# Optimization experiments

Measured on AMD Instinct MI355X. Metric: run time of the kernel, lower is better.

Reference implementation:

```python
import jax, jax.numpy as jnp
import numpy as np

NHEAD = 16


def corrcoef(X, Y):
    # X, Y: [..., S, D]; Pearson correlation between rows of X and rows of Y
    X = X - X.mean(-1, keepdims=True)
    Y = Y - Y.mean(-1, keepdims=True)
    c = jnp.einsum('...id,...jd->...ij', X, Y)            # [..., S, S]
    d = jnp.einsum('...id,...id->...i', X, Y)             # diagonal of c
    stddev = jnp.sqrt(d)
    c = c / stddev[..., :, None]
    c = c / stddev[..., None, :]
    c = jnp.clip(c, -1.0, 1.0)
    return jnp.where(jnp.isnan(c), 0.0, c)


def setup_inputs() -> dict:
    key = jax.random.key(0)
    k1, k2, k3 = jax.random.split(key, 3)
    T, B, D = 2048, 2, 1024
    query = jax.random.normal(k1, (T, B, D), dtype=jnp.float32)
    W_qkv = jax.random.normal(k2, (3 * D, D), dtype=jnp.float32) * (1.0 / np.sqrt(D))
    b_qkv = jax.random.normal(k3, (3 * D,), dtype=jnp.float32) * 0.01
    return {"query": query, "W_qkv": W_qkv, "b_qkv": b_qkv}


def reference(query, W_qkv, b_qkv):
    T, B, D = query.shape
    hd = D // NHEAD
    qkv = query @ W_qkv.T + b_qkv                          # [T, B, 3D]
    q, k, v = jnp.split(qkv, 3, axis=-1)

    def to_bhsd(x):
        return x.reshape(T, B, NHEAD, hd).transpose(1, 2, 0, 3)  # [B, H, S, hd]

    q, k, v = to_bhsd(q), to_bhsd(k), to_bhsd(v)
    corr = corrcoef(q, k)                                   # [B, H, S, S]
    corr = jax.nn.softmax(corr, axis=-1)                    # eval: dropout_p = 0
    return corr @ v                                         # [B, H, S, hd]
```

## Files before the change

kernel.cpp:

```cpp
#include <hip/hip_runtime.h>

#define S 2048
#define D 1024
#define NH 16
#define HD 64
#define N3 3072
#define M 4096

typedef short s16x8 __attribute__((ext_vector_type(8)));
typedef _Float16 f16x8 __attribute__((ext_vector_type(8)));
typedef float f32x4 __attribute__((ext_vector_type(4)));
typedef unsigned int u32;

__device__ __forceinline__ unsigned short f2bf(float f) {
  unsigned u = __builtin_bit_cast(unsigned, f);
  u += 0x7fffu + ((u >> 16) & 1u);
  return (unsigned short)(u >> 16);
}
__device__ __forceinline__ float bf2f(unsigned short h) {
  return __builtin_bit_cast(float, (unsigned)h << 16);
}

__device__ __forceinline__ float wsum(float v) {
  #pragma unroll
  for (int m = 1; m < 64; m <<= 1) v += __shfl_xor(v, m, 64);
  return v;
}

__device__ __forceinline__ void gload_lds16(const unsigned short* g, unsigned short* l) {
  __builtin_amdgcn_global_load_lds(
      (const __attribute__((address_space(1))) u32*)g,
      (__attribute__((address_space(3))) u32*)l, 16, 0, 0);
}

__global__ __launch_bounds__(256) void split_k(const float* __restrict__ q,
                                               const float* __restrict__ w,
                                               unsigned short* __restrict__ A1,
                                               unsigned short* __restrict__ A2,
                                               unsigned short* __restrict__ W1,
                                               unsigned short* __restrict__ W2) {
  const size_t gid = (size_t)blockIdx.x * 256 + threadIdx.x;
  const size_t NA = (size_t)M * D / 4;
  float4 x;
  unsigned short* p1; unsigned short* p2; size_t qi; float scale;
  if (gid < NA) {
    qi = gid;  x = ((const float4*)q)[qi];
    p1 = A1; p2 = A2; scale = 64.f;
  } else {
    qi = gid - NA;  x = ((const float4*)w)[qi];
    p1 = W1; p2 = W2; scale = 1024.f;
  }
  float e[4] = {x.x * scale, x.y * scale, x.z * scale, x.w * scale};
  unsigned short h1[4], h2[4];
  #pragma unroll
  for (int i = 0; i < 4; ++i) {
    _Float16 a = (_Float16)e[i];
    float r = e[i] - (float)a;
    _Float16 b = (_Float16)r;
    h1[i] = __builtin_bit_cast(unsigned short, a);
    h2[i] = __builtin_bit_cast(unsigned short, b);
  }
  *(ushort4*)&p1[qi * 4] = make_ushort4(h1[0], h1[1], h1[2], h1[3]);
  *(ushort4*)&p2[qi * 4] = make_ushort4(h2[0], h2[1], h2[2], h2[3]);
}

__global__ __launch_bounds__(256) void gemm_mfma(const unsigned short* __restrict__ A1,
                                                 const unsigned short* __restrict__ A2,
                                                 const unsigned short* __restrict__ W1,
                                                 const unsigned short* __restrict__ W2,
                                                 const float* __restrict__ bias,
                                                 float* __restrict__ C) {
  __shared__ unsigned short As[128 * 64];
  __shared__ unsigned short Bs[128 * 64];
  const int tid = threadIdx.x;
  const int w = tid >> 6, l = tid & 63;
  const int lo = l & 15, hi = l >> 4;
  const int n0 = blockIdx.x * 128, m0 = blockIdx.y * 128;
  const int wr = w >> 1, wc = w & 1;

  const int nseg = (n0 >= 2048) ? 1 : 3;

  const int srow = (tid >> 3) & 31;
  const int skc = tid & 7;

  f32x4 acc[4][4];
  #pragma unroll
  for (int mi = 0; mi < 4; ++mi)
    #pragma unroll
    for (int nj = 0; nj < 4; ++nj) acc[mi][nj] = (f32x4){0.f, 0.f, 0.f, 0.f};

  for (int s = 0; s < 3; ++s) {
    if (s >= nseg) break;
    const unsigned short* Ab;
    const unsigned short* Bb;
    switch (s) {
      case 0: Ab = A1; Bb = W1; break;
      case 1: Ab = A2; Bb = W1; break;
      default: Ab = A1; Bb = W2; break;
    }
    Ab += (size_t)m0 * D;
    Bb += (size_t)n0 * D;

    for (int k0 = 0; k0 < D; k0 += 64) {
      __syncthreads();
      #pragma unroll
      for (int c = 0; c < 4; ++c) {
        const int row = c * 32 + srow;
        const int koct = skc ^ (row & 7);
        gload_lds16(Ab + (size_t)row * D + k0 + koct * 8,
                    As + c * 2048 + w * 512);
        gload_lds16(Bb + (size_t)row * D + k0 + koct * 8,
                    Bs + c * 2048 + w * 512);
      }
      __syncthreads();

      f16x8 af[4][2], bf[4][2];
      #pragma unroll
      for (int mi = 0; mi < 4; ++mi)
        #pragma unroll
        for (int ks = 0; ks < 2; ++ks) {
          const int row = wr * 64 + mi * 16 + lo;
          const int koct = (ks * 4 + hi) ^ (lo & 7);
          af[mi][ks] = *(const f16x8*)&As[row * 64 + koct * 8];
        }
      #pragma unroll
      for (int nj = 0; nj < 4; ++nj)
        #pragma unroll
        for (int ks = 0; ks < 2; ++ks) {
          const int row = wc * 64 + nj * 16 + lo;
          const int koct = (ks * 4 + hi) ^ (lo & 7);
          bf[nj][ks] = *(const f16x8*)&Bs[row * 64 + koct * 8];
        }
      #pragma unroll
      for (int mi = 0; mi < 4; ++mi)
        #pragma unroll
        for (int nj = 0; nj < 4; ++nj)
          #pragma unroll
          for (int ks = 0; ks < 2; ++ks)
            acc[mi][nj] = __builtin_amdgcn_mfma_f32_16x16x32_f16(
                af[mi][ks], bf[nj][ks], acc[mi][nj], 0, 0, 0);
    }
  }

  #pragma unroll
  for (int mi = 0; mi < 4; ++mi)
    #pragma unroll
    for (int nj = 0; nj < 4; ++nj) {
      const int n = n0 + wc * 64 + nj * 16 + lo;
      const float bj = bias[n];
      #pragma unroll
      for (int r = 0; r < 4; ++r) {
        const int m = m0 + wr * 64 + mi * 16 + hi * 4 + r;
        C[(size_t)m * N3 + n] = acc[mi][nj][r] * (1.f / 65536.f) + bj;
      }
    }
}

__global__ __launch_bounds__(256) void stats_k(const float* __restrict__ qkv,
                                               unsigned short* __restrict__ qhi,
                                               unsigned short* __restrict__ qlo,
                                               unsigned short* __restrict__ khi,
                                               unsigned short* __restrict__ klo,
                                               unsigned short* __restrict__ vt,
                                               float* __restrict__ rs) {
  __shared__ unsigned short VsT[64][65];
  const int tt = blockIdx.x, bh = blockIdx.y;
  const int b = bh >> 4, h = bh & 15;
  const int w = threadIdx.x >> 6, l = threadIdx.x & 63;

  for (int rr = 0; rr < 16; ++rr) {
    const int t = tt * 64 + w * 16 + rr;
    const size_t base = (size_t)(t * 2 + b) * N3 + h * HD;
    const float q = qkv[base + l];
    const float k = qkv[base + D + l];
    const float v = qkv[base + 2 * D + l];
    const float qm = wsum(q) * (1.f / 64.f);
    const float km = wsum(k) * (1.f / 64.f);
    const float qcv = q - qm, kcv = k - km;
    const float d = wsum(qcv * kcv);
    float rv = 0.f;
    if (d > 0.f) {
      rv = rsqrtf(d);
      rv = rv * (1.5f - 0.5f * d * rv * rv);
    }
    const size_t ro = ((size_t)bh * S + t) * HD + l;
    const unsigned short qh = f2bf(qcv);
    const unsigned short kh = f2bf(kcv);
    qhi[ro] = qh;  qlo[ro] = f2bf(qcv - bf2f(qh));
    khi[ro] = kh;  klo[ro] = f2bf(kcv - bf2f(kh));
    if (l == 0) rs[(size_t)bh * S + t] = rv;
    VsT[l][w * 16 + rr] = f2bf(v);
  }
  __syncthreads();
  const int dd = threadIdx.x >> 2, seg = threadIdx.x & 3;
  unsigned pk[8];
  #pragma unroll
  for (int e = 0; e < 8; ++e) {
    unsigned l2 = VsT[dd][seg * 16 + 2 * e];
    unsigned h2 = VsT[dd][seg * 16 + 2 * e + 1];
    pk[e] = l2 | (h2 << 16);
  }
  unsigned short* dst = vt + ((size_t)bh * HD + dd) * S + tt * 64 + seg * 16;
  *(uint4*)dst       = make_uint4(pk[0], pk[1], pk[2], pk[3]);
  *(uint4*)(dst + 8) = make_uint4(pk[4], pk[5], pk[6], pk[7]);
}

__global__ __launch_bounds__(256) void attn_k(const unsigned short* __restrict__ qhi,
                                              const unsigned short* __restrict__ qlo,
                                              const unsigned short* __restrict__ khi,
                                              const unsigned short* __restrict__ klo,
                                              const unsigned short* __restrict__ vt,
                                              const float* __restrict__ rs,
                                              float* __restrict__ out) {
  __shared__ unsigned short Kh[64 * 64];
  __shared__ unsigned short Kl[64 * 64];
  __shared__ unsigned short Vsm[64 * 64];
  __shared__ unsigned short Ps[128 * 64];

  const int tid = threadIdx.x;
  const int w = tid >> 6, l = tid & 63;
  const int lo = l & 15, hi = l >> 4;

  const int wgid = blockIdx.x;
  const int orig = (wgid & 7) * 64 + (wgid >> 3);
  const int bh = orig >> 4, qt = orig & 15;

  const unsigned short* qhb = qhi + (size_t)bh * S * HD;
  const unsigned short* qlb = qlo + (size_t)bh * S * HD;
  const unsigned short* khb = khi + (size_t)bh * S * HD;
  const unsigned short* klb = klo + (size_t)bh * S * HD;
  const unsigned short* vbase = vt + (size_t)bh * HD * S;
  const float* rbase = rs + (size_t)bh * S;
  const int qrow0 = qt * 128 + w * 32;

  const int srow8 = l >> 3;
  const int sg = (l & 7) ^ srow8;

  s16x8 aqh[2][2], aql[2][2];
  #pragma unroll
  for (int mi = 0; mi < 2; ++mi)
    #pragma unroll
    for (int ks = 0; ks < 2; ++ks) {
      const size_t off = (size_t)(qrow0 + mi * 16 + lo) * HD + ks * 32 + hi * 8;
      aqh[mi][ks] = *(const s16x8*)(qhb + off);
      aql[mi][ks] = *(const s16x8*)(qlb + off);
    }

  float rsq[2][4];
  #pragma unroll
  for (int mi = 0; mi < 2; ++mi)
    #pragma unroll
    for (int r = 0; r < 4; ++r)
      rsq[mi][r] = rbase[qrow0 + mi * 16 + hi * 4 + r];

  f32x4 oacc[2][4];
  float den[2][4];
  #pragma unroll
  for (int mi = 0; mi < 2; ++mi)
    #pragma unroll
    for (int nd = 0; nd < 4; ++nd) {
      oacc[mi][nd] = (f32x4){0.f, 0.f, 0.f, 0.f};
      den[mi][nd] = 0.f;
    }

  for (int j0 = 0; j0 < S; j0 += 64) {
    __syncthreads();
    #pragma unroll
    for (int c = 0; c < 2; ++c) {
      const int row = c * 32 + w * 8 + srow8;
      const size_t kgo = (size_t)(j0 + row) * HD + sg * 8;
      const int dst = c * 2048 + w * 512;
      gload_lds16(khb + kgo, Kh + dst);
      gload_lds16(klb + kgo, Kl + dst);
      gload_lds16(vbase + (size_t)row * S + j0 + sg * 8, Vsm + dst);
    }
    float rjv[4];
    #pragma unroll
    for (int nj = 0; nj < 4; ++nj) rjv[nj] = rbase[j0 + nj * 16 + lo];
    __syncthreads();

    #pragma unroll
    for (int mi = 0; mi < 2; ++mi) {
      #pragma unroll
      for (int nj = 0; nj < 4; ++nj) {
        f32x4 acc = (f32x4){0.f, 0.f, 0.f, 0.f};
        #pragma unroll
        for (int ks = 0; ks < 2; ++ks) {
          const int off = (nj * 16 + lo) * 64 + (((ks * 4 + hi) ^ (lo & 7)) << 3);
          s16x8 bkh = *(const s16x8*)&Kh[off];
          s16x8 bkl = *(const s16x8*)&Kl[off];
          acc = __builtin_amdgcn_mfma_f32_16x16x32_bf16(aqh[mi][ks], bkh, acc, 0, 0, 0);
          acc = __builtin_amdgcn_mfma_f32_16x16x32_bf16(aqh[mi][ks], bkl, acc, 0, 0, 0);
          acc = __builtin_amdgcn_mfma_f32_16x16x32_bf16(aql[mi][ks], bkh, acc, 0, 0, 0);
        }
        #pragma unroll
        for (int r = 0; r < 4; ++r) {
          float c = acc[r] * rsq[mi][r] * rjv[nj];
          c = fminf(1.f, fmaxf(-1.f, c));
          const float e = __expf(c);
          den[mi][r] += e;
          const int pr = w * 32 + mi * 16 + hi * 4 + r;
          Ps[pr * 64 + ((((nj * 2) + (lo >> 3)) ^ (pr & 7)) << 3) + (lo & 7)] = f2bf(e);
        }
      }
    }

    #pragma unroll
    for (int mi = 0; mi < 2; ++mi) {
      const int prow = w * 32 + mi * 16 + lo;
      s16x8 pa0 = *(const s16x8*)&Ps[prow * 64 + ((hi ^ (lo & 7)) << 3)];
      s16x8 pa1 = *(const s16x8*)&Ps[prow * 64 + (((4 + hi) ^ (lo & 7)) << 3)];
      #pragma unroll
      for (int nd = 0; nd < 4; ++nd) {
        const int vrow = nd * 16 + lo;
        s16x8 bv0 = *(const s16x8*)&Vsm[vrow * 64 + ((hi ^ (lo & 7)) << 3)];
        s16x8 bv1 = *(const s16x8*)&Vsm[vrow * 64 + (((4 + hi) ^ (lo & 7)) << 3)];
        oacc[mi][nd] = __builtin_amdgcn_mfma_f32_16x16x32_bf16(pa0, bv0, oacc[mi][nd], 0, 0, 0);
        oacc[mi][nd] = __builtin_amdgcn_mfma_f32_16x16x32_bf16(pa1, bv1, oacc[mi][nd], 0, 0, 0);
      }
    }
  }

  #pragma unroll
  for (int mi = 0; mi < 2; ++mi)
    #pragma unroll
    for (int r = 0; r < 4; ++r) {
      float dsum = den[mi][r];
      dsum += __shfl_xor(dsum, 1, 64);
      dsum += __shfl_xor(dsum, 2, 64);
      dsum += __shfl_xor(dsum, 4, 64);
      dsum += __shfl_xor(dsum, 8, 64);
      den[mi][r] = 1.f / dsum;
    }
  #pragma unroll
  for (int mi = 0; mi < 2; ++mi)
    #pragma unroll
    for (int nd = 0; nd < 4; ++nd)
      #pragma unroll
      for (int r = 0; r < 4; ++r) {
        const size_t row = (size_t)bh * S + qrow0 + mi * 16 + hi * 4 + r;
        out[row * HD + nd * 16 + lo] = oacc[mi][nd][r] * den[mi][r];
      }
}

extern "C" void kernel_launch(void* const* d_in, const int* in_sizes, int n_in,
                              void* d_out, int out_size, void* d_ws, size_t ws_size,
                              hipStream_t stream) {
  const float* query = (const float*)d_in[0];
  const float* W     = (const float*)d_in[1];
  const float* bias  = (const float*)d_in[2];
  float* out = (float*)d_out;
  char* ws = (char*)d_ws;

  float*          qkv = (float*)ws;
  unsigned short* A1 = (unsigned short*)(ws + 50331648);
  unsigned short* A2 = (unsigned short*)(ws + 58720256);
  unsigned short* W1 = (unsigned short*)(ws + 67108864);
  unsigned short* W2 = (unsigned short*)(ws + 73400320);
  unsigned short* qhi = (unsigned short*)(ws + 50331648);
  unsigned short* qlo = (unsigned short*)(ws + 58720256);
  unsigned short* khi = (unsigned short*)(ws + 67108864);
  unsigned short* klo = (unsigned short*)(ws + 75497472);
  unsigned short* vt  = (unsigned short*)(ws + 83886080);
  float*          rsb = (float*)(ws + 92274688);

  split_k  <<<dim3(7168), 256, 0, stream>>>(query, W, A1, A2, W1, W2);
  gemm_mfma<<<dim3(24, 32), 256, 0, stream>>>(A1, A2, W1, W2, bias, qkv);
  stats_k  <<<dim3(32, 32), 256, 0, stream>>>(qkv, qhi, qlo, khi, klo, vt, rsb);
  attn_k   <<<dim3(512), 256, 0, stream>>>(qhi, qlo, khi, klo, vt, rsb, out);
}
```

Baseline: 192.4 us.

## Prescale q/k by row rstd and split attention across eight 16-row waves

The stats kernel now multiplies the centered q and k rows by the per-row reciprocal stddev before the bf16 hi/lo split. This lets the attention kernel drop the rs buffer, its per-tile loads and the per-element rescaling. The attention kernel moves to 512 threads, with each of 8 waves handling 16 query rows instead of 32, and each thread now issues a single K/V tile load. The goal is more resident waves and fewer registers per wave to hide latency, but each K/V fragment read from LDS now feeds half as many MFMAs.

```diff
diff --git a/kernel.cpp b/kernel.cpp
--- a/kernel.cpp
+++ b/kernel.cpp
@@ -161,8 +161,7 @@
                                                unsigned short* __restrict__ qlo,
                                                unsigned short* __restrict__ khi,
                                                unsigned short* __restrict__ klo,
-                                               unsigned short* __restrict__ vt,
-                                               float* __restrict__ rs) {
+                                               unsigned short* __restrict__ vt) {
   __shared__ unsigned short VsT[64][65];
   const int tt = blockIdx.x, bh = blockIdx.y;
   const int b = bh >> 4, h = bh & 15;
@@ -183,12 +182,12 @@
       rv = rsqrtf(d);
       rv = rv * (1.5f - 0.5f * d * rv * rv);
     }
+    const float qn = qcv * rv, kn = kcv * rv;
     const size_t ro = ((size_t)bh * S + t) * HD + l;
-    const unsigned short qh = f2bf(qcv);
-    const unsigned short kh = f2bf(kcv);
-    qhi[ro] = qh;  qlo[ro] = f2bf(qcv - bf2f(qh));
-    khi[ro] = kh;  klo[ro] = f2bf(kcv - bf2f(kh));
-    if (l == 0) rs[(size_t)bh * S + t] = rv;
+    const unsigned short qh = f2bf(qn);
+    const unsigned short kh = f2bf(kn);
+    qhi[ro] = qh;  qlo[ro] = f2bf(qn - bf2f(qh));
+    khi[ro] = kh;  klo[ro] = f2bf(kn - bf2f(kh));
     VsT[l][w * 16 + rr] = f2bf(v);
   }
   __syncthreads();
@@ -205,12 +204,11 @@
   *(uint4*)(dst + 8) = make_uint4(pk[4], pk[5], pk[6], pk[7]);
 }
 
-__global__ __launch_bounds__(256) void attn_k(const unsigned short* __restrict__ qhi,
+__global__ __launch_bounds__(512) void attn_k(const unsigned short* __restrict__ qhi,
                                               const unsigned short* __restrict__ qlo,
                                               const unsigned short* __restrict__ khi,
                                               const unsigned short* __restrict__ klo,
                                               const unsigned short* __restrict__ vt,
-                                              const float* __restrict__ rs,
                                               float* __restrict__ out) {
   __shared__ unsigned short Kh[64 * 64];
   __shared__ unsigned short Kl[64 * 64];
@@ -230,84 +228,58 @@
   const unsigned short* khb = khi + (size_t)bh * S * HD;
   const unsigned short* klb = klo + (size_t)bh * S * HD;
   const unsigned short* vbase = vt + (size_t)bh * HD * S;
-  const float* rbase = rs + (size_t)bh * S;
-  const int qrow0 = qt * 128 + w * 32;
-
-  const int srow8 = l >> 3;
-  const int sg = (l & 7) ^ srow8;
-
-  s16x8 aqh[2][2], aql[2][2];
-  #pragma unroll
-  for (int mi = 0; mi < 2; ++mi)
-    #pragma unroll
-    for (int ks = 0; ks < 2; ++ks) {
-      const size_t off = (size_t)(qrow0 + mi * 16 + lo) * HD + ks * 32 + hi * 8;
-      aqh[mi][ks] = *(const s16x8*)(qhb + off);
-      aql[mi][ks] = *(const s16x8*)(qlb + off);
-    }
-
-  float rsq[2][4];
-  #pragma unroll
-  for (int mi = 0; mi < 2; ++mi)
-    #pragma unroll
-    for (int r = 0; r < 4; ++r)
-      rsq[mi][r] = rbase[qrow0 + mi * 16 + hi * 4 + r];
-
-  f32x4 oacc[2][4];
-  float den[2][4];
-  #pragma unroll
-  for (int mi = 0; mi < 2; ++mi)
-    #pragma unroll
-    for (int nd = 0; nd < 4; ++nd) {
-      oacc[mi][nd] = (f32x4){0.f, 0.f, 0.f, 0.f};
-      den[mi][nd] = 0.f;
-    }
+  const int qrow0 = qt * 128 + w * 16;
+
+  const int srow = tid >> 3;
+  const int sg = (tid & 7) ^ (srow & 7);
+
+  s16x8 aqh[2], aql[2];
+  #pragma unroll
+  for (int ks = 0; ks < 2; ++ks) {
+    const size_t off = (size_t)(qrow0 + lo) * HD + ks * 32 + hi * 8;
+    aqh[ks] = *(const s16x8*)(qhb + off);
+    aql[ks] = *(const s16x8*)(qlb + off);
+  }
+
+  f32x4 oacc[4];
+  float den[4];
+  #pragma unroll
+  for (int nd = 0; nd < 4; ++nd) { oacc[nd] = (f32x4){0.f, 0.f, 0.f, 0.f}; den[nd] = 0.f; }
 
   for (int j0 = 0; j0 < S; j0 += 64) {
     __syncthreads();
+    {
+      const size_t kgo = (size_t)(j0 + srow) * HD + sg * 8;
+      gload_lds16(khb + kgo, Kh + w * 512);
+      gload_lds16(klb + kgo, Kl + w * 512);
+      gload_lds16(vbase + (size_t)srow * S + j0 + sg * 8, Vsm + w * 512);
+    }
+    __syncthreads();
+
     #pragma unroll
-    for (int c = 0; c < 2; ++c) {
-      const int row = c * 32 + w * 8 + srow8;
-      const size_t kgo = (size_t)(j0 + row) * HD + sg * 8;
-      const int dst = c * 2048 + w * 512;
-      gload_lds16(khb + kgo, Kh + dst);
-      gload_lds16(klb + kgo, Kl + dst);
-      gload_lds16(vbase + (size_t)row * S + j0 + sg * 8, Vsm + dst);
-    }
-    float rjv[4];
-    #pragma unroll
-    for (int nj = 0; nj < 4; ++nj) rjv[nj] = rbase[j0 + nj * 16 + lo];
-    __syncthreads();
-
-    #pragma unroll
-    for (int mi = 0; mi < 2; ++mi) {
-      #pragma unroll
-      for (int nj = 0; nj < 4; ++nj) {
-        f32x4 acc = (f32x4){0.f, 0.f, 0.f, 0.f};
-        #pragma unroll
-        for (int ks = 0; ks < 2; ++ks) {
-          const int off = (nj * 16 + lo) * 64 + (((ks * 4 + hi) ^ (lo & 7)) << 3);
-          s16x8 bkh = *(const s16x8*)&Kh[off];
-          s16x8 bkl = *(const s16x8*)&Kl[off];
-          acc = __builtin_amdgcn_mfma_f32_16x16x32_bf16(aqh[mi][ks], bkh, acc, 0, 0, 0);
-          acc = __builtin_amdgcn_mfma_f32_16x16x32_bf16(aqh[mi][ks], bkl, acc, 0, 0, 0);
-          acc = __builtin_amdgcn_mfma_f32_16x16x32_bf16(aql[mi][ks], bkh, acc, 0, 0, 0);
-        }
-        #pragma unroll
-        for (int r = 0; r < 4; ++r) {
-          float c = acc[r] * rsq[mi][r] * rjv[nj];
-          c = fminf(1.f, fmaxf(-1.f, c));
-          const float e = __expf(c);
-          den[mi][r] += e;
-          const int pr = w * 32 + mi * 16 + hi * 4 + r;
-          Ps[pr * 64 + ((((nj * 2) + (lo >> 3)) ^ (pr & 7)) << 3) + (lo & 7)] = f2bf(e);
-        }
-      }
-    }
-
-    #pragma unroll
-    for (int mi = 0; mi < 2; ++mi) {
-      const int prow = w * 32 + mi * 16 + lo;
+    for (int nj = 0; nj < 4; ++nj) {
+      f32x4 acc = (f32x4){0.f, 0.f, 0.f, 0.f};
+      #pragma unroll
+      for (int ks = 0; ks < 2; ++ks) {
+        const int off = (nj * 16 + lo) * 64 + (((ks * 4 + hi) ^ (lo & 7)) << 3);
+        s16x8 bkh = *(const s16x8*)&Kh[off];
+        s16x8 bkl = *(const s16x8*)&Kl[off];
+        acc = __builtin_amdgcn_mfma_f32_16x16x32_bf16(aqh[ks], bkh, acc, 0, 0, 0);
+        acc = __builtin_amdgcn_mfma_f32_16x16x32_bf16(aqh[ks], bkl, acc, 0, 0, 0);
+        acc = __builtin_amdgcn_mfma_f32_16x16x32_bf16(aql[ks], bkh, acc, 0, 0, 0);
+      }
+      #pragma unroll
+      for (int r = 0; r < 4; ++r) {
+        float c = fminf(1.f, fmaxf(-1.f, acc[r]));
+        const float e = __expf(c);
+        den[r] += e;
+        const int pr = w * 16 + hi * 4 + r;
+        Ps[pr * 64 + ((((nj * 2) + (lo >> 3)) ^ (pr & 7)) << 3) + (lo & 7)] = f2bf(e);
+      }
+    }
+
+    {
+      const int prow = w * 16 + lo;
       s16x8 pa0 = *(const s16x8*)&Ps[prow * 64 + ((hi ^ (lo & 7)) << 3)];
       s16x8 pa1 = *(const s16x8*)&Ps[prow * 64 + (((4 + hi) ^ (lo & 7)) << 3)];
       #pragma unroll
@@ -315,32 +287,28 @@
         const int vrow = nd * 16 + lo;
         s16x8 bv0 = *(const s16x8*)&Vsm[vrow * 64 + ((hi ^ (lo & 7)) << 3)];
         s16x8 bv1 = *(const s16x8*)&Vsm[vrow * 64 + (((4 + hi) ^ (lo & 7)) << 3)];
-        oacc[mi][nd] = __builtin_amdgcn_mfma_f32_16x16x32_bf16(pa0, bv0, oacc[mi][nd], 0, 0, 0);
-        oacc[mi][nd] = __builtin_amdgcn_mfma_f32_16x16x32_bf16(pa1, bv1, oacc[mi][nd], 0, 0, 0);
-      }
-    }
-  }
-
-  #pragma unroll
-  for (int mi = 0; mi < 2; ++mi)
+        oacc[nd] = __builtin_amdgcn_mfma_f32_16x16x32_bf16(pa0, bv0, oacc[nd], 0, 0, 0);
+        oacc[nd] = __builtin_amdgcn_mfma_f32_16x16x32_bf16(pa1, bv1, oacc[nd], 0, 0, 0);
+      }
+    }
+  }
+
+  #pragma unroll
+  for (int r = 0; r < 4; ++r) {
+    float dsum = den[r];
+    dsum += __shfl_xor(dsum, 1, 64);
+    dsum += __shfl_xor(dsum, 2, 64);
+    dsum += __shfl_xor(dsum, 4, 64);
+    dsum += __shfl_xor(dsum, 8, 64);
+    den[r] = 1.f / dsum;
+  }
+  #pragma unroll
+  for (int nd = 0; nd < 4; ++nd)
     #pragma unroll
     for (int r = 0; r < 4; ++r) {
-      float dsum = den[mi][r];
-      dsum += __shfl_xor(dsum, 1, 64);
-      dsum += __shfl_xor(dsum, 2, 64);
-      dsum += __shfl_xor(dsum, 4, 64);
-      dsum += __shfl_xor(dsum, 8, 64);
-      den[mi][r] = 1.f / dsum;
-    }
-  #pragma unroll
-  for (int mi = 0; mi < 2; ++mi)
-    #pragma unroll
-    for (int nd = 0; nd < 4; ++nd)
-      #pragma unroll
-      for (int r = 0; r < 4; ++r) {
-        const size_t row = (size_t)bh * S + qrow0 + mi * 16 + hi * 4 + r;
-        out[row * HD + nd * 16 + lo] = oacc[mi][nd][r] * den[mi][r];
-      }
+      const size_t row = (size_t)bh * S + qrow0 + hi * 4 + r;
+      out[row * HD + nd * 16 + lo] = oacc[nd][r] * den[r];
+    }
 }
 
 extern "C" void kernel_launch(void* const* d_in, const int* in_sizes, int n_in,
@@ -362,10 +330,9 @@
   unsigned short* khi = (unsigned short*)(ws + 67108864);
   unsigned short* klo = (unsigned short*)(ws + 75497472);
   unsigned short* vt  = (unsigned short*)(ws + 83886080);
-  float*          rsb = (float*)(ws + 92274688);
 
   split_k  <<<dim3(7168), 256, 0, stream>>>(query, W, A1, A2, W1, W2);
   gemm_mfma<<<dim3(24, 32), 256, 0, stream>>>(A1, A2, W1, W2, bias, qkv);
-  stats_k  <<<dim3(32, 32), 256, 0, stream>>>(qkv, qhi, qlo, khi, klo, vt, rsb);
-  attn_k   <<<dim3(512), 256, 0, stream>>>(qhi, qlo, khi, klo, vt, rsb, out);
-}
+  stats_k  <<<dim3(32, 32), 256, 0, stream>>>(qkv, qhi, qlo, khi, klo, vt);
+  attn_k   <<<dim3(512), 512, 0, stream>>>(qhi, qlo, khi, klo, vt, out);
+}
```

Result: faster. 177.7 us (-7.6%).

## Keep softmax probabilities in registers using transposed 32x32 MFMA and fp16 V

Applied to the files above, without the earlier changes.

Rewrites the attention inner loop to use 32x32x16 MFMAs that compute S^T (K as the A operand, Q as B). The exponentiated probabilities are then packed to fp16 and redistributed with a cross-half-wave shuffle so they feed the PV MFMA directly from registers, with no round trip through the Ps shared-memory buffer. V is now stored as fp16 instead of bf16 to match, and the per-column row scales are loaded into LDS once per tile. This removes the LDS writes and reads for P and one barrier-free bank-conflict source, at the cost of extra shuffles and a changed output write pattern.

```diff
diff --git a/kernel.cpp b/kernel.cpp
--- a/kernel.cpp
+++ b/kernel.cpp
@@ -10,7 +10,9 @@
 typedef short s16x8 __attribute__((ext_vector_type(8)));
 typedef _Float16 f16x8 __attribute__((ext_vector_type(8)));
 typedef float f32x4 __attribute__((ext_vector_type(4)));
+typedef float f32x16 __attribute__((ext_vector_type(16)));
 typedef unsigned int u32;
+typedef u32 u32x4 __attribute__((ext_vector_type(4)));
 
 __device__ __forceinline__ unsigned short f2bf(float f) {
   unsigned u = __builtin_bit_cast(unsigned, f);
@@ -20,6 +22,10 @@
 __device__ __forceinline__ float bf2f(unsigned short h) {
   return __builtin_bit_cast(float, (unsigned)h << 16);
 }
+__device__ __forceinline__ unsigned short f2h(float f) {
+  _Float16 h = (_Float16)f;
+  return __builtin_bit_cast(unsigned short, h);
+}
 
 __device__ __forceinline__ float wsum(float v) {
   #pragma unroll
@@ -31,6 +37,11 @@
   __builtin_amdgcn_global_load_lds(
       (const __attribute__((address_space(1))) u32*)g,
       (__attribute__((address_space(3))) u32*)l, 16, 0, 0);
+}
+__device__ __forceinline__ void gload_lds4(const float* g, float* l) {
+  __builtin_amdgcn_global_load_lds(
+      (const __attribute__((address_space(1))) u32*)g,
+      (__attribute__((address_space(3))) u32*)l, 4, 0, 0);
 }
 
 __global__ __launch_bounds__(256) void split_k(const float* __restrict__ q,
@@ -189,7 +200,7 @@
     qhi[ro] = qh;  qlo[ro] = f2bf(qcv - bf2f(qh));
     khi[ro] = kh;  klo[ro] = f2bf(kcv - bf2f(kh));
     if (l == 0) rs[(size_t)bh * S + t] = rv;
-    VsT[l][w * 16 + rr] = f2bf(v);
+    VsT[l][w * 16 + rr] = f2h(v);
   }
   __syncthreads();
   const int dd = threadIdx.x >> 2, seg = threadIdx.x & 3;
@@ -215,11 +226,13 @@
   __shared__ unsigned short Kh[64 * 64];
   __shared__ unsigned short Kl[64 * 64];
   __shared__ unsigned short Vsm[64 * 64];
-  __shared__ unsigned short Ps[128 * 64];
+  __shared__ float Rsl[64];
 
   const int tid = threadIdx.x;
   const int w = tid >> 6, l = tid & 63;
-  const int lo = l & 15, hi = l >> 4;
+  const int lq = l & 31;
+  const int h = l >> 5;
+  const int l7 = l & 7;
 
   const int wgid = blockIdx.x;
   const int orig = (wgid & 7) * 64 + (wgid >> 3);
@@ -233,114 +246,103 @@
   const float* rbase = rs + (size_t)bh * S;
   const int qrow0 = qt * 128 + w * 32;
 
-  const int srow8 = l >> 3;
-  const int sg = (l & 7) ^ srow8;
-
-  s16x8 aqh[2][2], aql[2][2];
-  #pragma unroll
-  for (int mi = 0; mi < 2; ++mi)
-    #pragma unroll
-    for (int ks = 0; ks < 2; ++ks) {
-      const size_t off = (size_t)(qrow0 + mi * 16 + lo) * HD + ks * 32 + hi * 8;
-      aqh[mi][ks] = *(const s16x8*)(qhb + off);
-      aql[mi][ks] = *(const s16x8*)(qlb + off);
-    }
-
-  float rsq[2][4];
-  #pragma unroll
-  for (int mi = 0; mi < 2; ++mi)
-    #pragma unroll
-    for (int r = 0; r < 4; ++r)
-      rsq[mi][r] = rbase[qrow0 + mi * 16 + hi * 4 + r];
-
-  f32x4 oacc[2][4];
-  float den[2][4];
-  #pragma unroll
-  for (int mi = 0; mi < 2; ++mi)
-    #pragma unroll
-    for (int nd = 0; nd < 4; ++nd) {
-      oacc[mi][nd] = (f32x4){0.f, 0.f, 0.f, 0.f};
-      den[mi][nd] = 0.f;
-    }
+  const int srow3 = l >> 3;
+  const int sg = l7 ^ srow3;
+
+  s16x8 qfh[4], qfl[4];
+  #pragma unroll
+  for (int kc = 0; kc < 4; ++kc) {
+    const size_t off = (size_t)(qrow0 + lq) * HD + kc * 16 + h * 8;
+    qfh[kc] = *(const s16x8*)(qhb + off);
+    qfl[kc] = *(const s16x8*)(qlb + off);
+  }
+  const float rsq = rbase[qrow0 + lq];
+
+  f32x16 oacc[2];
+  oacc[0] = (f32x16)(0.f);
+  oacc[1] = (f32x16)(0.f);
+  float den = 0.f;
 
   for (int j0 = 0; j0 < S; j0 += 64) {
     __syncthreads();
     #pragma unroll
     for (int c = 0; c < 2; ++c) {
-      const int row = c * 32 + w * 8 + srow8;
-      const size_t kgo = (size_t)(j0 + row) * HD + sg * 8;
+      const int row = c * 32 + w * 8 + srow3;
       const int dst = c * 2048 + w * 512;
-      gload_lds16(khb + kgo, Kh + dst);
-      gload_lds16(klb + kgo, Kl + dst);
+      gload_lds16(khb + (size_t)(j0 + row) * HD + sg * 8, Kh + dst);
+      gload_lds16(klb + (size_t)(j0 + row) * HD + sg * 8, Kl + dst);
       gload_lds16(vbase + (size_t)row * S + j0 + sg * 8, Vsm + dst);
     }
-    float rjv[4];
-    #pragma unroll
-    for (int nj = 0; nj < 4; ++nj) rjv[nj] = rbase[j0 + nj * 16 + lo];
+    if (w == 0) gload_lds4(rbase + j0 + l, Rsl);
     __syncthreads();
 
     #pragma unroll
-    for (int mi = 0; mi < 2; ++mi) {
-      #pragma unroll
-      for (int nj = 0; nj < 4; ++nj) {
-        f32x4 acc = (f32x4){0.f, 0.f, 0.f, 0.f};
+    for (int jblk = 0; jblk < 2; ++jblk) {
+      f32x16 sacc = (f32x16)(0.f);
+      #pragma unroll
+      for (int kc = 0; kc < 4; ++kc) {
+        const int off = (jblk * 32 + lq) * 64 + (((kc * 2 + h) ^ l7) << 3);
+        s16x8 akh = *(const s16x8*)&Kh[off];
+        s16x8 akl = *(const s16x8*)&Kl[off];
+        sacc = __builtin_amdgcn_mfma_f32_32x32x16_bf16(akh, qfh[kc], sacc, 0, 0, 0);
+        sacc = __builtin_amdgcn_mfma_f32_32x32x16_bf16(akl, qfh[kc], sacc, 0, 0, 0);
+        sacc = __builtin_amdgcn_mfma_f32_32x32x16_bf16(akh, qfl[kc], sacc, 0, 0, 0);
+      }
+
+      u32 pkA[4], pkB[4];
+      #pragma unroll
+      for (int g = 0; g < 4; ++g) {
+        f32x4 rjv = *(const f32x4*)&Rsl[jblk * 32 + g * 8 + h * 4];
+        float e0, e1, e2, e3;
+        {
+          float c0 = fminf(1.f, fmaxf(-1.f, sacc[4 * g + 0] * rsq * rjv[0]));
+          float c1 = fminf(1.f, fmaxf(-1.f, sacc[4 * g + 1] * rsq * rjv[1]));
+          float c2 = fminf(1.f, fmaxf(-1.f, sacc[4 * g + 2] * rsq * rjv[2]));
+          float c3 = fminf(1.f, fmaxf(-1.f, sacc[4 * g + 3] * rsq * rjv[3]));
+          e0 = __expf(c0); e1 = __expf(c1); e2 = __expf(c2); e3 = __expf(c3);
+        }
+        den += (e0 + e1) + (e2 + e3);
+        pkA[g] = __builtin_bit_cast(u32, __builtin_amdgcn_cvt_pkrtz(e0, e1));
+        pkB[g] = __builtin_bit_cast(u32, __builtin_amdgcn_cvt_pkrtz(e2, e3));
+      }
+
+      #pragma unroll
+      for (int jc2 = 0; jc2 < 2; ++jc2) {
+        const u32 sA = h ? pkA[2 * jc2] : pkA[2 * jc2 + 1];
+        const u32 sB = h ? pkB[2 * jc2] : pkB[2 * jc2 + 1];
+        const u32 rA = (u32)__shfl_xor((int)sA, 32, 64);
+        const u32 rB = (u32)__shfl_xor((int)sB, 32, 64);
+        u32x4 uu;
+        uu[0] = h ? rA : pkA[2 * jc2];
+        uu[1] = h ? rB : pkB[2 * jc2];
+        uu[2] = h ? pkA[2 * jc2 + 1] : rA;
+        uu[3] = h ? pkB[2 * jc2 + 1] : rB;
+        const f16x8 pa = __builtin_bit_cast(f16x8, uu);
+
+        const int jcg = jblk * 2 + jc2;
         #pragma unroll
-        for (int ks = 0; ks < 2; ++ks) {
-          const int off = (nj * 16 + lo) * 64 + (((ks * 4 + hi) ^ (lo & 7)) << 3);
-          s16x8 bkh = *(const s16x8*)&Kh[off];
-          s16x8 bkl = *(const s16x8*)&Kl[off];
-          acc = __builtin_amdgcn_mfma_f32_16x16x32_bf16(aqh[mi][ks], bkh, acc, 0, 0, 0);
-          acc = __builtin_amdgcn_mfma_f32_16x16x32_bf16(aqh[mi][ks], bkl, acc, 0, 0, 0);
-          acc = __builtin_amdgcn_mfma_f32_16x16x32_bf16(aql[mi][ks], bkh, acc, 0, 0, 0);
+        for (int dblk = 0; dblk < 2; ++dblk) {
+          const int voff = (dblk * 32 + lq) * 64 + (((jcg * 2 + h) ^ l7) << 3);
+          f16x8 bv = *(const f16x8*)&Vsm[voff];
+          oacc[dblk] = __builtin_amdgcn_mfma_f32_32x32x16_f16(pa, bv, oacc[dblk], 0, 0, 0);
         }
-        #pragma unroll
-        for (int r = 0; r < 4; ++r) {
-          float c = acc[r] * rsq[mi][r] * rjv[nj];
-          c = fminf(1.f, fmaxf(-1.f, c));
-          const float e = __expf(c);
-          den[mi][r] += e;
-          const int pr = w * 32 + mi * 16 + hi * 4 + r;
-          Ps[pr * 64 + ((((nj * 2) + (lo >> 3)) ^ (pr & 7)) << 3) + (lo & 7)] = f2bf(e);
-        }
-      }
-    }
-
-    #pragma unroll
-    for (int mi = 0; mi < 2; ++mi) {
-      const int prow = w * 32 + mi * 16 + lo;
-      s16x8 pa0 = *(const s16x8*)&Ps[prow * 64 + ((hi ^ (lo & 7)) << 3)];
-      s16x8 pa1 = *(const s16x8*)&Ps[prow * 64 + (((4 + hi) ^ (lo & 7)) << 3)];
-      #pragma unroll
-      for (int nd = 0; nd < 4; ++nd) {
-        const int vrow = nd * 16 + lo;
-        s16x8 bv0 = *(const s16x8*)&Vsm[vrow * 64 + ((hi ^ (lo & 7)) << 3)];
-        s16x8 bv1 = *(const s16x8*)&Vsm[vrow * 64 + (((4 + hi) ^ (lo & 7)) << 3)];
-        oacc[mi][nd] = __builtin_amdgcn_mfma_f32_16x16x32_bf16(pa0, bv0, oacc[mi][nd], 0, 0, 0);
-        oacc[mi][nd] = __builtin_amdgcn_mfma_f32_16x16x32_bf16(pa1, bv1, oacc[mi][nd], 0, 0, 0);
-      }
-    }
-  }
-
-  #pragma unroll
-  for (int mi = 0; mi < 2; ++mi)
-    #pragma unroll
-    for (int r = 0; r < 4; ++r) {
-      float dsum = den[mi][r];
-      dsum += __shfl_xor(dsum, 1, 64);
-      dsum += __shfl_xor(dsum, 2, 64);
-      dsum += __shfl_xor(dsum, 4, 64);
-      dsum += __shfl_xor(dsum, 8, 64);
-      den[mi][r] = 1.f / dsum;
-    }
-  #pragma unroll
-  for (int mi = 0; mi < 2; ++mi)
-    #pragma unroll
-    for (int nd = 0; nd < 4; ++nd)
-      #pragma unroll
-      for (int r = 0; r < 4; ++r) {
-        const size_t row = (size_t)bh * S + qrow0 + mi * 16 + hi * 4 + r;
-        out[row * HD + nd * 16 + lo] = oacc[mi][nd][r] * den[mi][r];
-      }
+      }
+    }
+  }
+
+  const float dtot = den + __shfl_xor(den, 32, 64);
+  const float inv = 1.f / dtot;
+
+  #pragma unroll
+  for (int g = 0; g < 4; ++g)
+    #pragma unroll
+    for (int i = 0; i < 4; ++i) {
+      const int qr = i + 8 * g + 4 * h;
+      const float invq = __shfl(inv, i + 8 * g + 4 * h, 64);
+      const size_t row = (size_t)bh * S + qrow0 + qr;
+      out[row * HD + lq]      = oacc[0][4 * g + i] * invq;
+      out[row * HD + 32 + lq] = oacc[1][4 * g + i] * invq;
+    }
 }
 
 extern "C" void kernel_launch(void* const* d_in, const int* in_sizes, int n_in,
```

Measured after the change: 184.5 us. -4.1%, faster.
